# Performance work log

Hardware: AMD Instinct MI355X
Metric: run time of the kernel (lower is better)

## Reference

```python
import jax, jax.numpy as jnp
import numpy as np

D_MODEL = 768
HEADS = 12
D_K = D_MODEL // HEADS


def setup_inputs() -> dict:
    key = jax.random.key(0)
    ks = jax.random.split(key, 11)
    B, S = 2, 2048
    scale = 1.0 / np.sqrt(D_MODEL)
    inp = {
        "q": jax.random.normal(ks[0], (B, S, D_MODEL), jnp.float32),
        "k": jax.random.normal(ks[1], (B, S, D_MODEL), jnp.float32),
        "v": jax.random.normal(ks[2], (B, S, D_MODEL), jnp.float32),
        "Wq": jax.random.normal(ks[3], (D_MODEL, D_MODEL), jnp.float32) * scale,
        "bq": jnp.zeros((D_MODEL,), jnp.float32),
        "Wk": jax.random.normal(ks[4], (D_MODEL, D_MODEL), jnp.float32) * scale,
        "bk": jnp.zeros((D_MODEL,), jnp.float32),
        "Wv": jax.random.normal(ks[5], (D_MODEL, D_MODEL), jnp.float32) * scale,
        "bv": jnp.zeros((D_MODEL,), jnp.float32),
        "Wo": jax.random.normal(ks[6], (D_MODEL, D_MODEL), jnp.float32) * scale,
        "bo": jnp.zeros((D_MODEL,), jnp.float32),
    }
    return inp


def reference(q, k, v, Wq, bq, Wk, bk, Wv, bv, Wo, bo):
    B, S, _ = q.shape
    # linear projections, then split heads: [B, H, S, Dk]
    def proj(x, W, b):
        y = jnp.einsum('bsd,df->bsf', x, W) + b
        return y.reshape(B, -1, HEADS, D_K).transpose(0, 2, 1, 3)
    qh = proj(q, Wq, bq)
    kh = proj(k, Wk, bk)
    vh = proj(v, Wv, bv)
    scores = jnp.einsum('bhqd,bhkd->bhqk', qh, kh) / jnp.sqrt(jnp.float32(D_K))
    attn = jax.nn.softmax(scores, axis=-1)  # dropout is identity at eval
    out = jnp.einsum('bhqk,bhkd->bhqd', attn, vh)
    out = out.transpose(0, 2, 1, 3).reshape(B, -1, D_MODEL)
    return jnp.einsum('bsd,df->bsf', out, Wo) + bo
```

## Files before the change

### kernel.cpp

```cpp
#include <hip/hip_runtime.h>
#include <hip/hip_bf16.h>
#include <stdint.h>

#define DMODEL 768
#define NHEADS 12
#define DK 64
#define BATCH 2
#define SEQ 2048

typedef __attribute__((ext_vector_type(8))) short shortx8;
typedef __attribute__((ext_vector_type(4))) float f32x4;
typedef __attribute__((ext_vector_type(8))) __bf16 bf16v8;

static __device__ __forceinline__ ushort f2bf(float f) {
  __bf16 b = (__bf16)f;
  ushort u;
  __builtin_memcpy(&u, &b, 2);
  return u;
}
static __device__ __forceinline__ float bf2f(ushort u) {
  __bf16 b;
  __builtin_memcpy(&b, &u, 2);
  return (float)b;
}

template <typename AB>
static __device__ __forceinline__ auto mfma_impl(AB a, AB b, f32x4 c, int)
    -> decltype(__builtin_amdgcn_mfma_f32_16x16x32_bf16(a, b, c, 0, 0, 0)) {
  return __builtin_amdgcn_mfma_f32_16x16x32_bf16(a, b, c, 0, 0, 0);
}
template <typename AB>
static __device__ __forceinline__ f32x4 mfma_impl(AB a, AB b, f32x4 c, long) {
  bf16v8 av, bv;
  __builtin_memcpy(&av, &a, 16);
  __builtin_memcpy(&bv, &b, 16);
  return __builtin_amdgcn_mfma_f32_16x16x32_bf16(av, bv, c, 0, 0, 0);
}
static __device__ __forceinline__ f32x4 MFMA(shortx8 a, shortx8 b, f32x4 c) {
  return mfma_impl(a, b, c, 0);
}

typedef __attribute__((address_space(1))) void gvoid;
typedef __attribute__((address_space(3))) void lvoid;
static __device__ __forceinline__ void gload16(const void* g, void* lds) {
  __builtin_amdgcn_global_load_lds((gvoid*)g, (lvoid*)lds, 16, 0, 0);
}

__global__ __launch_bounds__(256) void wsplit_kernel(
    const float* __restrict__ W0, const float* __restrict__ W1,
    const float* __restrict__ W2, const float* __restrict__ W3,
    ushort* __restrict__ hiT, ushort* __restrict__ loT) {
  __shared__ float tile[32][33];
  const int wsel = blockIdx.z;
  const float* W = wsel == 0 ? W0 : wsel == 1 ? W1 : wsel == 2 ? W2 : W3;
  const int k0 = blockIdx.x * 32, n0 = blockIdx.y * 32;
  const int tx = threadIdx.x & 31, ty = threadIdx.x >> 5;
#pragma unroll
  for (int i = 0; i < 4; i++) {
    int kl = ty + i * 8;
    tile[kl][tx] = W[(size_t)(k0 + kl) * DMODEL + n0 + tx];
  }
  __syncthreads();
  ushort* hi = hiT + (size_t)wsel * DMODEL * DMODEL;
  ushort* lo = loT + (size_t)wsel * DMODEL * DMODEL;
#pragma unroll
  for (int i = 0; i < 4; i++) {
    int nl = ty + i * 8;
    float x = tile[tx][nl];
    ushort h = f2bf(x);
    ushort lw = f2bf(x - bf2f(h));
    hi[(size_t)(n0 + nl) * DMODEL + k0 + tx] = h;
    lo[(size_t)(n0 + nl) * DMODEL + k0 + tx] = lw;
  }
}

__global__ __launch_bounds__(256) void xconv_kernel(const float* __restrict__ q,
                                                    const float* __restrict__ k,
                                                    const float* __restrict__ v,
                                                    ushort* __restrict__ Xb) {
  const int z = blockIdx.z;
  const float* X = z == 0 ? q : z == 1 ? k : v;
  size_t i = ((size_t)blockIdx.x * 256 + threadIdx.x) * 8;
  float4 f0 = *(const float4*)&X[i];
  float4 f1 = *(const float4*)&X[i + 4];
  float xv[8] = {f0.x, f0.y, f0.z, f0.w, f1.x, f1.y, f1.z, f1.w};
  uint hw[4];
#pragma unroll
  for (int j = 0; j < 4; j++)
    hw[j] = (uint)f2bf(xv[2 * j]) | ((uint)f2bf(xv[2 * j + 1]) << 16);
  *(uint4*)&Xb[(size_t)z * 3145728 + i] = make_uint4(hw[0], hw[1], hw[2], hw[3]);
}

__global__ __launch_bounds__(256) void gemm_qkv(
    const ushort* __restrict__ Xb, const ushort* __restrict__ WTh,
    const float* __restrict__ bq, const float* __restrict__ bk,
    const float* __restrict__ bv, ushort* __restrict__ Qb,
    ushort* __restrict__ Kb, ushort* __restrict__ Vb) {
  __shared__ ushort sA[2][128 * 32];
  __shared__ ushort sB[2][128 * 32];
  const int t = threadIdx.x, l = t & 63, w = t >> 6;
  const int lr = l & 15, lg = l >> 4;
  const int wr = w >> 1, wc = w & 1;
  const int m0 = blockIdx.y * 128, n0 = blockIdx.x * 128;
  const int z = blockIdx.z;
  const ushort* A = Xb + (size_t)z * 3145728;
  const ushort* B = WTh + (size_t)z * 589824;

  const int srow_l = l >> 2;
  const int schunk = (l & 3) ^ ((l >> 3) & 3);
  auto stage = [&](int bi, int kk) {
#pragma unroll
    for (int i = 0; i < 2; i++) {
      int row = i * 64 + w * 16 + srow_l;
      gload16(&A[(size_t)(m0 + row) * DMODEL + kk + schunk * 8],
              &sA[bi][(i * 64 + w * 16) * 32]);
      gload16(&B[(size_t)(n0 + row) * DMODEL + kk + schunk * 8],
              &sB[bi][(i * 64 + w * 16) * 32]);
    }
  };

  f32x4 acc[4][4] = {};
  stage(0, 0);
  int cur = 0;
  const int rphys = (lg ^ ((lr >> 1) & 3)) * 8;
  for (int kk = 0; kk < DMODEL; kk += 32) {
    __syncthreads();
    if (kk + 32 < DMODEL) stage(cur ^ 1, kk + 32);
    shortx8 af[4], bf_[4];
#pragma unroll
    for (int ti = 0; ti < 4; ti++)
      af[ti] = *(const shortx8*)&sA[cur][(wr * 64 + ti * 16 + lr) * 32 + rphys];
#pragma unroll
    for (int tj = 0; tj < 4; tj++)
      bf_[tj] = *(const shortx8*)&sB[cur][(wc * 64 + tj * 16 + lr) * 32 + rphys];
    __builtin_amdgcn_s_setprio(1);
#pragma unroll
    for (int ti = 0; ti < 4; ti++)
#pragma unroll
      for (int tj = 0; tj < 4; tj++)
        acc[ti][tj] = MFMA(af[ti], bf_[tj], acc[ti][tj]);
    __builtin_amdgcn_s_setprio(0);
    cur ^= 1;
  }

  const float* bias = z == 0 ? bq : z == 1 ? bk : bv;
  ushort* out = z == 0 ? Qb : z == 1 ? Kb : Vb;
  const float sc_ = z == 0 ? 0.125f : 1.0f;
#pragma unroll
  for (int ti = 0; ti < 4; ti++)
#pragma unroll
    for (int tj = 0; tj < 4; tj++) {
      int n = n0 + wc * 64 + tj * 16 + lr;
      float bv_ = bias[n];
      int hd = n >> 6, dd = n & 63;
#pragma unroll
      for (int rr = 0; rr < 4; rr++) {
        int m = m0 + wr * 64 + ti * 16 + lg * 4 + rr;
        int bb = m >> 11, s = m & 2047;
        float y = (acc[ti][tj][rr] + bv_) * sc_;
        out[(((size_t)(bb * NHEADS + hd)) * SEQ + s) * DK + dd] = f2bf(y);
      }
    }
}

__global__ __launch_bounds__(256) void vtrans_kernel(const ushort* __restrict__ V,
                                                     ushort* __restrict__ VT) {
  __shared__ ushort tl[64][72];
  const int t = threadIdx.x;
  const int s0 = blockIdx.x * 64, h = blockIdx.y, b = blockIdx.z;
  const size_t ib = ((size_t)(b * NHEADS + h)) * SEQ * DK;
  const size_t ob = ((size_t)(b * NHEADS + h)) * DK * SEQ;
#pragma unroll
  for (int i = 0; i < 2; i++) {
    int c = i * 256 + t, row = c >> 3, off = (c & 7) * 8;
    *(uint4*)&tl[row][off] = *(const uint4*)&V[ib + (size_t)(s0 + row) * DK + off];
  }
  __syncthreads();
#pragma unroll
  for (int i = 0; i < 2; i++) {
    int c = i * 256 + t, d = c >> 3, so = (c & 7) * 8;
    ushort tmp[8];
#pragma unroll
    for (int j = 0; j < 8; j++) tmp[j] = tl[so + j][d];
    *(uint4*)&VT[ob + (size_t)d * SEQ + s0 + so] = *(uint4*)tmp;
  }
}

__global__ __launch_bounds__(256) void attn_kernel(
    const ushort* __restrict__ Qb, const ushort* __restrict__ Kb,
    const ushort* __restrict__ VTb, ushort* __restrict__ Oh,
    ushort* __restrict__ Ol) {
  __shared__ ushort Ksh[2][64 * 64];
  __shared__ ushort Vsh[2][64 * 64];
  __shared__ ushort Psh[4][16 * 72];
  const int t = threadIdx.x, l = t & 63, w = t >> 6;
  const int lr = l & 15, lg = l >> 4;
  const int s0 = blockIdx.x * 64, h = blockIdx.y, b = blockIdx.z;
  const size_t bh = ((size_t)(b * NHEADS + h)) * SEQ * DK;
  const size_t vt = ((size_t)(b * NHEADS + h)) * DK * SEQ;
  ushort* Pw = Psh[w];

  const int kchunk = ((l & 7) ^ (l >> 3)) * 8;
  auto stageKV = [&](int bi, int sk) {
#pragma unroll
    for (int i = 0; i < 2; i++) {
      int r = i * 32 + w * 8 + (l >> 3);
      gload16(&Kb[bh + (size_t)(sk + r) * DK + kchunk],
              &Ksh[bi][(i * 32 + w * 8) * 64]);
      gload16(&VTb[vt + (size_t)r * SEQ + sk + kchunk],
              &Vsh[bi][(i * 32 + w * 8) * 64]);
    }
  };

  shortx8 qf0, qf1;
  {
    size_t qrow = bh + (size_t)(s0 + w * 16 + lr) * DK;
    qf0 = *(const shortx8*)&Qb[qrow + lg * 8];
    qf1 = *(const shortx8*)&Qb[qrow + 32 + lg * 8];
  }
  f32x4 oacc[4] = {};
  float mrun = -1e30f, lrun = 0.f;

  stageKV(0, 0);
  int cur = 0;
  const int p0 = (lg ^ (lr & 7)) * 8;
  const int p1 = ((lg + 4) ^ (lr & 7)) * 8;
  for (int sk = 0; sk < SEQ; sk += 64) {
    __syncthreads();
    if (sk + 64 < SEQ) stageKV(cur ^ 1, sk + 64);

    f32x4 sc[4];
    __builtin_amdgcn_s_setprio(1);
#pragma unroll
    for (int kt = 0; kt < 4; kt++) {
      int rb = (kt * 16 + lr) * 64;
      shortx8 kh0 = *(const shortx8*)&Ksh[cur][rb + p0];
      shortx8 kh1 = *(const shortx8*)&Ksh[cur][rb + p1];
      f32x4 s_ = {};
      s_ = MFMA(kh0, qf0, s_);
      s_ = MFMA(kh1, qf1, s_);
      sc[kt] = s_;
    }
    __builtin_amdgcn_s_setprio(0);

    float vmax = fmaxf(
        fmaxf(fmaxf(fmaxf(sc[0][0], sc[0][1]), fmaxf(sc[0][2], sc[0][3])),
              fmaxf(fmaxf(sc[1][0], sc[1][1]), fmaxf(sc[1][2], sc[1][3]))),
        fmaxf(fmaxf(fmaxf(sc[2][0], sc[2][1]), fmaxf(sc[2][2], sc[2][3])),
              fmaxf(fmaxf(sc[3][0], sc[3][1]), fmaxf(sc[3][2], sc[3][3]))));
    vmax = fmaxf(vmax, __shfl_xor(vmax, 16));
    vmax = fmaxf(vmax, __shfl_xor(vmax, 32));
    if (__any(vmax > mrun + 8.0f)) {
      float mnew = fmaxf(mrun, vmax);
      float fac = __expf(mrun - mnew);
      mrun = mnew;
      lrun *= fac;
#pragma unroll
      for (int rr = 0; rr < 4; rr++) {
        float fr = __shfl(fac, lg * 4 + rr, 16);
#pragma unroll
        for (int dt = 0; dt < 4; dt++) oacc[dt][rr] *= fr;
      }
    }
    float psum = 0.f;
#pragma unroll
    for (int kt = 0; kt < 4; kt++)
#pragma unroll
      for (int r = 0; r < 4; r++) {
        float p = __expf(sc[kt][r] - mrun);
        sc[kt][r] = p;
        psum += p;
      }
    psum += __shfl_xor(psum, 16);
    psum += __shfl_xor(psum, 32);
    lrun += psum;

#pragma unroll
    for (int kt = 0; kt < 4; kt++) {
      uint u0 = (uint)f2bf(sc[kt][0]) | ((uint)f2bf(sc[kt][1]) << 16);
      uint u1 = (uint)f2bf(sc[kt][2]) | ((uint)f2bf(sc[kt][3]) << 16);
      *(uint2*)&Pw[lr * 72 + kt * 16 + lg * 4] = make_uint2(u0, u1);
    }
    asm volatile("s_waitcnt lgkmcnt(0)" ::: "memory");
    __builtin_amdgcn_sched_barrier(0);
    shortx8 pa0 = *(const shortx8*)&Pw[lr * 72 + lg * 8];
    shortx8 pa1 = *(const shortx8*)&Pw[lr * 72 + 32 + lg * 8];

    __builtin_amdgcn_s_setprio(1);
#pragma unroll
    for (int dt = 0; dt < 4; dt++) {
      int rb = (dt * 16 + lr) * 64;
      shortx8 vb0 = *(const shortx8*)&Vsh[cur][rb + p0];
      shortx8 vb1 = *(const shortx8*)&Vsh[cur][rb + p1];
      oacc[dt] = MFMA(pa0, vb0, oacc[dt]);
      oacc[dt] = MFMA(pa1, vb1, oacc[dt]);
    }
    __builtin_amdgcn_s_setprio(0);
    cur ^= 1;
  }

  float linv = 1.0f / lrun;
#pragma unroll
  for (int rr = 0; rr < 4; rr++) {
    float li = __shfl(linv, lg * 4 + rr, 16);
    int s = s0 + w * 16 + lg * 4 + rr;
    size_t orow = ((size_t)b * SEQ + s) * DMODEL + h * DK;
#pragma unroll
    for (int dt = 0; dt < 4; dt++) {
      float y = oacc[dt][rr] * li;
      ushort hh = f2bf(y);
      Oh[orow + dt * 16 + lr] = hh;
      Ol[orow + dt * 16 + lr] = f2bf(y - bf2f(hh));
    }
  }
}

__global__ __launch_bounds__(256) void gemm_out(
    const ushort* __restrict__ AH, const ushort* __restrict__ AL,
    const ushort* __restrict__ BH, const ushort* __restrict__ BL,
    const float* __restrict__ bias, float* __restrict__ outF) {
  __shared__ ushort sAh[2][128 * 32], sAl[2][128 * 32];
  __shared__ ushort sBh[2][64 * 32], sBl[2][64 * 32];
  const int t = threadIdx.x, l = t & 63, w = t >> 6;
  const int lr = l & 15, lg = l >> 4;
  const int m0 = blockIdx.y * 128, n0 = blockIdx.x * 64;

  const int srow_l = l >> 2;
  const int schunk = (l & 3) ^ ((l >> 3) & 3);
  auto stage = [&](int bi, int kk) {
#pragma unroll
    for (int i = 0; i < 2; i++) {
      int row = i * 64 + w * 16 + srow_l;
      size_t ga = (size_t)(m0 + row) * DMODEL + kk + schunk * 8;
      gload16(&AH[ga], &sAh[bi][(i * 64 + w * 16) * 32]);
      gload16(&AL[ga], &sAl[bi][(i * 64 + w * 16) * 32]);
    }
    {
      int row = w * 16 + srow_l;
      size_t gb = (size_t)(n0 + row) * DMODEL + kk + schunk * 8;
      gload16(&BH[gb], &sBh[bi][(w * 16) * 32]);
      gload16(&BL[gb], &sBl[bi][(w * 16) * 32]);
    }
  };

  f32x4 acc[2][4] = {};
  stage(0, 0);
  int cur = 0;
  const int rphys = (lg ^ ((lr >> 1) & 3)) * 8;
  for (int kk = 0; kk < DMODEL; kk += 32) {
    __syncthreads();
    if (kk + 32 < DMODEL) stage(cur ^ 1, kk + 32);
    shortx8 ah[2], al_[2], bh[4], bl[4];
#pragma unroll
    for (int ti = 0; ti < 2; ti++) {
      int r = (w * 32 + ti * 16 + lr) * 32 + rphys;
      ah[ti] = *(const shortx8*)&sAh[cur][r];
      al_[ti] = *(const shortx8*)&sAl[cur][r];
    }
#pragma unroll
    for (int tj = 0; tj < 4; tj++) {
      int r = (tj * 16 + lr) * 32 + rphys;
      bh[tj] = *(const shortx8*)&sBh[cur][r];
      bl[tj] = *(const shortx8*)&sBl[cur][r];
    }
    __builtin_amdgcn_s_setprio(1);
#pragma unroll
    for (int ti = 0; ti < 2; ti++)
#pragma unroll
      for (int tj = 0; tj < 4; tj++) {
        acc[ti][tj] = MFMA(ah[ti], bh[tj], acc[ti][tj]);
        acc[ti][tj] = MFMA(ah[ti], bl[tj], acc[ti][tj]);
        acc[ti][tj] = MFMA(al_[ti], bh[tj], acc[ti][tj]);
      }
    __builtin_amdgcn_s_setprio(0);
    cur ^= 1;
  }

#pragma unroll
  for (int ti = 0; ti < 2; ti++)
#pragma unroll
    for (int tj = 0; tj < 4; tj++) {
      int n = n0 + tj * 16 + lr;
      float bv_ = bias[n];
#pragma unroll
      for (int rr = 0; rr < 4; rr++) {
        int m = m0 + w * 32 + ti * 16 + lg * 4 + rr;
        outF[(size_t)m * DMODEL + n] = acc[ti][tj][rr] + bv_;
      }
    }
}

extern "C" void kernel_launch(void* const* d_in, const int* in_sizes, int n_in,
                              void* d_out, int out_size, void* d_ws,
                              size_t ws_size, hipStream_t stream) {
  const float* q = (const float*)d_in[0];
  const float* k = (const float*)d_in[1];
  const float* v = (const float*)d_in[2];
  const float* Wq = (const float*)d_in[3];
  const float* bq = (const float*)d_in[4];
  const float* Wk = (const float*)d_in[5];
  const float* bk = (const float*)d_in[6];
  const float* Wv = (const float*)d_in[7];
  const float* bv = (const float*)d_in[8];
  const float* Wo = (const float*)d_in[9];
  const float* bo = (const float*)d_in[10];
  float* out = (float*)d_out;

  constexpr size_t WMAT = (size_t)DMODEL * DMODEL;
  constexpr size_t XMAT = (size_t)BATCH * SEQ * DMODEL;

  ushort* WTh = (ushort*)d_ws;
  ushort* WTl = WTh + 4 * WMAT;
  ushort* Xb = WTl + 4 * WMAT;
  ushort* Qb = Xb + 3 * XMAT;
  ushort* Kb = Qb + XMAT;
  ushort* Vb = Kb + XMAT;
  ushort* VTb = Vb + XMAT;
  ushort* Oh = Xb;
  ushort* Ol = Xb + XMAT;

  wsplit_kernel<<<dim3(24, 24, 4), 256, 0, stream>>>(Wq, Wk, Wv, Wo, WTh, WTl);
  xconv_kernel<<<dim3(1536, 1, 3), 256, 0, stream>>>(q, k, v, Xb);
  gemm_qkv<<<dim3(6, 32, 3), 256, 0, stream>>>(Xb, WTh, bq, bk, bv, Qb, Kb, Vb);
  vtrans_kernel<<<dim3(SEQ / 64, NHEADS, BATCH), 256, 0, stream>>>(Vb, VTb);
  attn_kernel<<<dim3(SEQ / 64, NHEADS, BATCH), 256, 0, stream>>>(Qb, Kb, VTb,
                                                                 Oh, Ol);
  gemm_out<<<dim3(12, 32, 1), 256, 0, stream>>>(Oh, Ol, WTh + 3 * WMAT,
                                                WTl + 3 * WMAT, bo, out);
}
```

Baseline: 228.7 us.

## Switch pipeline from bf16 split-precision to fp16 single-pass MFMA with exp2 softmax

Replaces bf16 storage and MFMA with fp16 throughout the pipeline. This removes the hi/lo split of the weights and of the attention output, so the output projection runs one MFMA per tile instead of three and loads half the operand data. The softmax now uses exp2 with log2(e) folded into the Q scale, plus a packed fp16 conversion for P. The risk is fp16 range and overflow on activations, and lower accuracy in the output GEMM now that the error-compensating split is gone.

```diff
diff --git a/kernel.cpp b/kernel.cpp
--- a/kernel.cpp
+++ b/kernel.cpp
@@ -10,34 +10,43 @@
 
 typedef __attribute__((ext_vector_type(8))) short shortx8;
 typedef __attribute__((ext_vector_type(4))) float f32x4;
-typedef __attribute__((ext_vector_type(8))) __bf16 bf16v8;
-
-static __device__ __forceinline__ ushort f2bf(float f) {
-  __bf16 b = (__bf16)f;
+typedef __attribute__((ext_vector_type(8))) _Float16 half8;
+
+static __device__ __forceinline__ ushort f2h(float f) {
+  _Float16 h = (_Float16)f;
   ushort u;
-  __builtin_memcpy(&u, &b, 2);
+  __builtin_memcpy(&u, &h, 2);
   return u;
 }
-static __device__ __forceinline__ float bf2f(ushort u) {
-  __bf16 b;
-  __builtin_memcpy(&b, &u, 2);
-  return (float)b;
+static __device__ __forceinline__ uint pk2h(float a, float b) {
+  auto h = __builtin_amdgcn_cvt_pkrtz(a, b);
+  uint u;
+  __builtin_memcpy(&u, &h, 4);
+  return u;
+}
+static __device__ __forceinline__ float exp2_fast(float x) {
+  float r;
+  asm("v_exp_f32 %0, %1" : "=v"(r) : "v"(x));
+  return r;
 }
 
 template <typename AB>
-static __device__ __forceinline__ auto mfma_impl(AB a, AB b, f32x4 c, int)
-    -> decltype(__builtin_amdgcn_mfma_f32_16x16x32_bf16(a, b, c, 0, 0, 0)) {
-  return __builtin_amdgcn_mfma_f32_16x16x32_bf16(a, b, c, 0, 0, 0);
+static __device__ __forceinline__ auto mfma16_impl(AB a, AB b, f32x4 c, int)
+    -> decltype(__builtin_amdgcn_mfma_f32_16x16x32_f16(a, b, c, 0, 0, 0)) {
+  return __builtin_amdgcn_mfma_f32_16x16x32_f16(a, b, c, 0, 0, 0);
 }
 template <typename AB>
-static __device__ __forceinline__ f32x4 mfma_impl(AB a, AB b, f32x4 c, long) {
-  bf16v8 av, bv;
+static __device__ __forceinline__ f32x4 mfma16_impl(AB a, AB b, f32x4 c, long) {
+  shortx8 av, bv;
   __builtin_memcpy(&av, &a, 16);
   __builtin_memcpy(&bv, &b, 16);
-  return __builtin_amdgcn_mfma_f32_16x16x32_bf16(av, bv, c, 0, 0, 0);
+  return __builtin_amdgcn_mfma_f32_16x16x32_f16(av, bv, c, 0, 0, 0);
 }
 static __device__ __forceinline__ f32x4 MFMA(shortx8 a, shortx8 b, f32x4 c) {
-  return mfma_impl(a, b, c, 0);
+  half8 ah, bh;
+  __builtin_memcpy(&ah, &a, 16);
+  __builtin_memcpy(&bh, &b, 16);
+  return mfma16_impl(ah, bh, c, 0);
 }
 
 typedef __attribute__((address_space(1))) void gvoid;
@@ -46,10 +55,10 @@
   __builtin_amdgcn_global_load_lds((gvoid*)g, (lvoid*)lds, 16, 0, 0);
 }
 
-__global__ __launch_bounds__(256) void wsplit_kernel(
+__global__ __launch_bounds__(256) void wconv_kernel(
     const float* __restrict__ W0, const float* __restrict__ W1,
     const float* __restrict__ W2, const float* __restrict__ W3,
-    ushort* __restrict__ hiT, ushort* __restrict__ loT) {
+    ushort* __restrict__ WT) {
   __shared__ float tile[32][33];
   const int wsel = blockIdx.z;
   const float* W = wsel == 0 ? W0 : wsel == 1 ? W1 : wsel == 2 ? W2 : W3;
@@ -61,16 +70,11 @@
     tile[kl][tx] = W[(size_t)(k0 + kl) * DMODEL + n0 + tx];
   }
   __syncthreads();
-  ushort* hi = hiT + (size_t)wsel * DMODEL * DMODEL;
-  ushort* lo = loT + (size_t)wsel * DMODEL * DMODEL;
+  ushort* o = WT + (size_t)wsel * DMODEL * DMODEL;
 #pragma unroll
   for (int i = 0; i < 4; i++) {
     int nl = ty + i * 8;
-    float x = tile[tx][nl];
-    ushort h = f2bf(x);
-    ushort lw = f2bf(x - bf2f(h));
-    hi[(size_t)(n0 + nl) * DMODEL + k0 + tx] = h;
-    lo[(size_t)(n0 + nl) * DMODEL + k0 + tx] = lw;
+    o[(size_t)(n0 + nl) * DMODEL + k0 + tx] = f2h(tile[tx][nl]);
   }
 }
 
@@ -83,16 +87,16 @@
   size_t i = ((size_t)blockIdx.x * 256 + threadIdx.x) * 8;
   float4 f0 = *(const float4*)&X[i];
   float4 f1 = *(const float4*)&X[i + 4];
-  float xv[8] = {f0.x, f0.y, f0.z, f0.w, f1.x, f1.y, f1.z, f1.w};
   uint hw[4];
-#pragma unroll
-  for (int j = 0; j < 4; j++)
-    hw[j] = (uint)f2bf(xv[2 * j]) | ((uint)f2bf(xv[2 * j + 1]) << 16);
+  hw[0] = (uint)f2h(f0.x) | ((uint)f2h(f0.y) << 16);
+  hw[1] = (uint)f2h(f0.z) | ((uint)f2h(f0.w) << 16);
+  hw[2] = (uint)f2h(f1.x) | ((uint)f2h(f1.y) << 16);
+  hw[3] = (uint)f2h(f1.z) | ((uint)f2h(f1.w) << 16);
   *(uint4*)&Xb[(size_t)z * 3145728 + i] = make_uint4(hw[0], hw[1], hw[2], hw[3]);
 }
 
 __global__ __launch_bounds__(256) void gemm_qkv(
-    const ushort* __restrict__ Xb, const ushort* __restrict__ WTh,
+    const ushort* __restrict__ Xb, const ushort* __restrict__ WT,
     const float* __restrict__ bq, const float* __restrict__ bk,
     const float* __restrict__ bv, ushort* __restrict__ Qb,
     ushort* __restrict__ Kb, ushort* __restrict__ Vb) {
@@ -104,7 +108,7 @@
   const int m0 = blockIdx.y * 128, n0 = blockIdx.x * 128;
   const int z = blockIdx.z;
   const ushort* A = Xb + (size_t)z * 3145728;
-  const ushort* B = WTh + (size_t)z * 589824;
+  const ushort* B = WT + (size_t)z * 589824;
 
   const int srow_l = l >> 2;
   const int schunk = (l & 3) ^ ((l >> 3) & 3);
@@ -145,7 +149,7 @@
 
   const float* bias = z == 0 ? bq : z == 1 ? bk : bv;
   ushort* out = z == 0 ? Qb : z == 1 ? Kb : Vb;
-  const float sc_ = z == 0 ? 0.125f : 1.0f;
+  const float sc_ = z == 0 ? 0.125f * 1.44269504f : 1.0f;
 #pragma unroll
   for (int ti = 0; ti < 4; ti++)
 #pragma unroll
@@ -158,7 +162,7 @@
         int m = m0 + wr * 64 + ti * 16 + lg * 4 + rr;
         int bb = m >> 11, s = m & 2047;
         float y = (acc[ti][tj][rr] + bv_) * sc_;
-        out[(((size_t)(bb * NHEADS + hd)) * SEQ + s) * DK + dd] = f2bf(y);
+        out[(((size_t)(bb * NHEADS + hd)) * SEQ + s) * DK + dd] = f2h(y);
       }
     }
 }
@@ -188,8 +192,7 @@
 
 __global__ __launch_bounds__(256) void attn_kernel(
     const ushort* __restrict__ Qb, const ushort* __restrict__ Kb,
-    const ushort* __restrict__ VTb, ushort* __restrict__ Oh,
-    ushort* __restrict__ Ol) {
+    const ushort* __restrict__ VTb, ushort* __restrict__ Ob) {
   __shared__ ushort Ksh[2][64 * 64];
   __shared__ ushort Vsh[2][64 * 64];
   __shared__ ushort Psh[4][16 * 72];
@@ -252,7 +255,7 @@
     vmax = fmaxf(vmax, __shfl_xor(vmax, 32));
     if (__any(vmax > mrun + 8.0f)) {
       float mnew = fmaxf(mrun, vmax);
-      float fac = __expf(mrun - mnew);
+      float fac = exp2_fast(mrun - mnew);
       mrun = mnew;
       lrun *= fac;
 #pragma unroll
@@ -267,7 +270,7 @@
     for (int kt = 0; kt < 4; kt++)
 #pragma unroll
       for (int r = 0; r < 4; r++) {
-        float p = __expf(sc[kt][r] - mrun);
+        float p = exp2_fast(sc[kt][r] - mrun);
         sc[kt][r] = p;
         psum += p;
       }
@@ -277,8 +280,8 @@
 
 #pragma unroll
     for (int kt = 0; kt < 4; kt++) {
-      uint u0 = (uint)f2bf(sc[kt][0]) | ((uint)f2bf(sc[kt][1]) << 16);
-      uint u1 = (uint)f2bf(sc[kt][2]) | ((uint)f2bf(sc[kt][3]) << 16);
+      uint u0 = pk2h(sc[kt][0], sc[kt][1]);
+      uint u1 = pk2h(sc[kt][2], sc[kt][3]);
       *(uint2*)&Pw[lr * 72 + kt * 16 + lg * 4] = make_uint2(u0, u1);
     }
     asm volatile("s_waitcnt lgkmcnt(0)" ::: "memory");
@@ -306,21 +309,16 @@
     int s = s0 + w * 16 + lg * 4 + rr;
     size_t orow = ((size_t)b * SEQ + s) * DMODEL + h * DK;
 #pragma unroll
-    for (int dt = 0; dt < 4; dt++) {
-      float y = oacc[dt][rr] * li;
-      ushort hh = f2bf(y);
-      Oh[orow + dt * 16 + lr] = hh;
-      Ol[orow + dt * 16 + lr] = f2bf(y - bf2f(hh));
-    }
+    for (int dt = 0; dt < 4; dt++)
+      Ob[orow + dt * 16 + lr] = f2h(oacc[dt][rr] * li);
   }
 }
 
 __global__ __launch_bounds__(256) void gemm_out(
-    const ushort* __restrict__ AH, const ushort* __restrict__ AL,
-    const ushort* __restrict__ BH, const ushort* __restrict__ BL,
+    const ushort* __restrict__ A, const ushort* __restrict__ B,
     const float* __restrict__ bias, float* __restrict__ outF) {
-  __shared__ ushort sAh[2][128 * 32], sAl[2][128 * 32];
-  __shared__ ushort sBh[2][64 * 32], sBl[2][64 * 32];
+  __shared__ ushort sA[2][128 * 32];
+  __shared__ ushort sB[2][64 * 32];
   const int t = threadIdx.x, l = t & 63, w = t >> 6;
   const int lr = l & 15, lg = l >> 4;
   const int m0 = blockIdx.y * 128, n0 = blockIdx.x * 64;
@@ -331,15 +329,13 @@
 #pragma unroll
     for (int i = 0; i < 2; i++) {
       int row = i * 64 + w * 16 + srow_l;
-      size_t ga = (size_t)(m0 + row) * DMODEL + kk + schunk * 8;
-      gload16(&AH[ga], &sAh[bi][(i * 64 + w * 16) * 32]);
-      gload16(&AL[ga], &sAl[bi][(i * 64 + w * 16) * 32]);
+      gload16(&A[(size_t)(m0 + row) * DMODEL + kk + schunk * 8],
+              &sA[bi][(i * 64 + w * 16) * 32]);
     }
     {
       int row = w * 16 + srow_l;
-      size_t gb = (size_t)(n0 + row) * DMODEL + kk + schunk * 8;
-      gload16(&BH[gb], &sBh[bi][(w * 16) * 32]);
-      gload16(&BL[gb], &sBl[bi][(w * 16) * 32]);
+      gload16(&B[(size_t)(n0 + row) * DMODEL + kk + schunk * 8],
+              &sB[bi][(w * 16) * 32]);
     }
   };
 
@@ -350,28 +346,19 @@
   for (int kk = 0; kk < DMODEL; kk += 32) {
     __syncthreads();
     if (kk + 32 < DMODEL) stage(cur ^ 1, kk + 32);
-    shortx8 ah[2], al_[2], bh[4], bl[4];
-#pragma unroll
-    for (int ti = 0; ti < 2; ti++) {
-      int r = (w * 32 + ti * 16 + lr) * 32 + rphys;
-      ah[ti] = *(const shortx8*)&sAh[cur][r];
-      al_[ti] = *(const shortx8*)&sAl[cur][r];
-    }
-#pragma unroll
-    for (int tj = 0; tj < 4; tj++) {
-      int r = (tj * 16 + lr) * 32 + rphys;
-      bh[tj] = *(const shortx8*)&sBh[cur][r];
-      bl[tj] = *(const shortx8*)&sBl[cur][r];
-    }
+    shortx8 af[2], bf_[4];
+#pragma unroll
+    for (int ti = 0; ti < 2; ti++)
+      af[ti] = *(const shortx8*)&sA[cur][(w * 32 + ti * 16 + lr) * 32 + rphys];
+#pragma unroll
+    for (int tj = 0; tj < 4; tj++)
+      bf_[tj] = *(const shortx8*)&sB[cur][(tj * 16 + lr) * 32 + rphys];
     __builtin_amdgcn_s_setprio(1);
 #pragma unroll
     for (int ti = 0; ti < 2; ti++)
 #pragma unroll
-      for (int tj = 0; tj < 4; tj++) {
-        acc[ti][tj] = MFMA(ah[ti], bh[tj], acc[ti][tj]);
-        acc[ti][tj] = MFMA(ah[ti], bl[tj], acc[ti][tj]);
-        acc[ti][tj] = MFMA(al_[ti], bh[tj], acc[ti][tj]);
-      }
+      for (int tj = 0; tj < 4; tj++)
+        acc[ti][tj] = MFMA(af[ti], bf_[tj], acc[ti][tj]);
     __builtin_amdgcn_s_setprio(0);
     cur ^= 1;
   }
@@ -409,22 +396,19 @@
   constexpr size_t WMAT = (size_t)DMODEL * DMODEL;
   constexpr size_t XMAT = (size_t)BATCH * SEQ * DMODEL;
 
-  ushort* WTh = (ushort*)d_ws;
-  ushort* WTl = WTh + 4 * WMAT;
-  ushort* Xb = WTl + 4 * WMAT;
+  ushort* WT = (ushort*)d_ws;
+  ushort* Xb = WT + 4 * WMAT;
   ushort* Qb = Xb + 3 * XMAT;
   ushort* Kb = Qb + XMAT;
   ushort* Vb = Kb + XMAT;
   ushort* VTb = Vb + XMAT;
-  ushort* Oh = Xb;
-  ushort* Ol = Xb + XMAT;
-
-  wsplit_kernel<<<dim3(24, 24, 4), 256, 0, stream>>>(Wq, Wk, Wv, Wo, WTh, WTl);
+  ushort* Ob = Xb;
+
+  wconv_kernel<<<dim3(24, 24, 4), 256, 0, stream>>>(Wq, Wk, Wv, Wo, WT);
   xconv_kernel<<<dim3(1536, 1, 3), 256, 0, stream>>>(q, k, v, Xb);
-  gemm_qkv<<<dim3(6, 32, 3), 256, 0, stream>>>(Xb, WTh, bq, bk, bv, Qb, Kb, Vb);
+  gemm_qkv<<<dim3(6, 32, 3), 256, 0, stream>>>(Xb, WT, bq, bk, bv, Qb, Kb, Vb);
   vtrans_kernel<<<dim3(SEQ / 64, NHEADS, BATCH), 256, 0, stream>>>(Vb, VTb);
   attn_kernel<<<dim3(SEQ / 64, NHEADS, BATCH), 256, 0, stream>>>(Qb, Kb, VTb,
-                                                                 Oh, Ol);
-  gemm_out<<<dim3(12, 32, 1), 256, 0, stream>>>(Oh, Ol, WTh + 3 * WMAT,
-                                                WTl + 3 * WMAT, bo, out);
-}
+                                                                 Ob);
+  gemm_out<<<dim3(12, 32, 1), 256, 0, stream>>>(Ob, WT + 3 * WMAT, bo, out);
+}
```

After: 209.4 us. -8.4%, faster.
